# Optimization experiments

Hardware: AMD Instinct MI355X
Metric: run time of the kernel (lower is better)

Reference implementation:

```python
import jax, jax.numpy as jnp
import numpy as np

D = 768
H = 12
B, T = 2, 2048


def _layernorm(x, g, b, eps=1e-5):
    m = jnp.mean(x, axis=-1, keepdims=True)
    v = jnp.mean((x - m) ** 2, axis=-1, keepdims=True)
    return (x - m) * jax.lax.rsqrt(v + eps) * g + b


def setup_inputs() -> dict:
    key = jax.random.key(0)
    ks = jax.random.split(key, 10)
    s = 0.02
    return {
        "x": jax.random.normal(ks[0], (B, T, D), dtype=jnp.float32),
        "attn_mask": jnp.ones((B, T), dtype=jnp.int32),
        "Wq": jax.random.normal(ks[1], (D, D), dtype=jnp.float32) * s,
        "Wk": jax.random.normal(ks[2], (D, D), dtype=jnp.float32) * s,
        "Wv": jax.random.normal(ks[3], (D, D), dtype=jnp.float32) * s,
        "Wo": jax.random.normal(ks[4], (D, D), dtype=jnp.float32) * s,
        "bo": jnp.zeros((D,), dtype=jnp.float32),
        "ln1_g": jnp.ones((D,), dtype=jnp.float32),
        "ln1_b": jnp.zeros((D,), dtype=jnp.float32),
        "ln2_g": jnp.ones((D,), dtype=jnp.float32),
        "ln2_b": jnp.zeros((D,), dtype=jnp.float32),
        "W1": jax.random.normal(ks[5], (D, 4 * D), dtype=jnp.float32) * s,
        "b1": jnp.zeros((4 * D,), dtype=jnp.float32),
        "W2": jax.random.normal(ks[6], (4 * D, D), dtype=jnp.float32) * s,
        "b2": jnp.zeros((D,), dtype=jnp.float32),
    }


def reference(x, attn_mask, Wq, Wk, Wv, Wo, bo, ln1_g, ln1_b, ln2_g, ln2_b, W1, b1, W2, b2):
    d = x.shape[-1]
    hs = d // H
    # --- multi-head self-attention on ln1(x) ---
    h = _layernorm(x, ln1_g, ln1_b)
    q = jnp.einsum("btd,dhk->bhtk", h, Wq.reshape(d, H, hs))
    k = jnp.einsum("btd,dhk->bhtk", h, Wk.reshape(d, H, hs))
    v = jnp.einsum("btd,dhk->bhtk", h, Wv.reshape(d, H, hs))
    # NOTE: original scales by embed_dim**-0.5 (C = embed_dim), not head_size
    scores = jnp.einsum("bhtk,bhsk->bhts", q, k) * (d ** -0.5)
    key_mask = (attn_mask == 0)[:, None, None, :]  # [B,1,1,T] over key dim
    scores = jnp.where(key_mask, -jnp.inf, scores)
    wei = jax.nn.softmax(scores, axis=-1)
    out = jnp.einsum("bhts,bhsk->bhtk", wei, v)
    out = out.transpose(0, 2, 1, 3).reshape(x.shape)  # concat heads -> [B,T,D]
    x = x + out @ Wo + bo
    # --- feed-forward on ln2(x) ---
    h2 = _layernorm(x, ln2_g, ln2_b)
    ff = jax.nn.relu(h2 @ W1 + b1) @ W2 + b2
    return x + ff
```

## Files before the change

kernel.cpp:

```cpp
#include <hip/hip_runtime.h>
#include <hip/hip_bf16.h>


typedef unsigned short u16;
typedef unsigned int u32;
typedef __attribute__((ext_vector_type(8))) short s16x8;
typedef __attribute__((ext_vector_type(4))) short s16x4;
typedef __attribute__((ext_vector_type(4))) float fx4;

#define D_MODEL 768
#define NH 12
#define HS 64
#define TT 2048
#define BB 2

__device__ __forceinline__ u16 f2bf(float f) {
  union { float f; u32 u; } v; v.f = f;
  u32 r = v.u + 0x7fffu + ((v.u >> 16) & 1u);
  return (u16)(r >> 16);
}
__device__ __forceinline__ float bf2f(u16 h) {
  union { u32 u; float f; } v; v.u = ((u32)h) << 16; return v.f;
}
__device__ __forceinline__ s16x4 pack4(float a, float b, float c, float d) {
  union { __hip_bfloat162 h2[2]; s16x4 v; } u;
  u.h2[0] = __float22bfloat162_rn({a, b});
  u.h2[1] = __float22bfloat162_rn({c, d});
  return u.v;
}

__device__ __forceinline__ void async16(const void* g, void* l) {
  __builtin_amdgcn_global_load_lds(
      (const __attribute__((address_space(1))) u32*)g,
      (__attribute__((address_space(3))) u32*)l, 16, 0, 0);
}

__device__ __forceinline__ s16x4 lds_rd64(const u16* base, int row, int g) {
  int a = row * 64 + ((((g >> 1) ^ (row & 7)) << 3) | ((g & 1) << 2));
  return *(const s16x4*)(base + a);
}

__global__ __launch_bounds__(256) void tconv(const float* __restrict__ in,
                                             u16* __restrict__ out, int R, int C) {
  __shared__ float t[32][33];
  int c0 = blockIdx.x * 32, r0 = blockIdx.y * 32;
  int x = threadIdx.x, y = threadIdx.y;
  for (int i = 0; i < 4; i++)
    t[y + i * 8][x] = in[(size_t)(r0 + y + i * 8) * C + c0 + x];
  __syncthreads();
  for (int i = 0; i < 4; i++)
    out[(size_t)(c0 + y + i * 8) * R + r0 + x] = f2bf(t[x][y + i * 8]);
}

__global__ __launch_bounds__(256) void tconv3(const float* __restrict__ w0,
                                              const float* __restrict__ w1,
                                              const float* __restrict__ w2,
                                              u16* __restrict__ out) {
  __shared__ float t[32][33];
  const float* in = blockIdx.z == 0 ? w0 : blockIdx.z == 1 ? w1 : w2;
  u16* o = out + (size_t)blockIdx.z * 768 * 768;
  int c0 = blockIdx.x * 32, r0 = blockIdx.y * 32;
  int x = threadIdx.x, y = threadIdx.y;
  for (int i = 0; i < 4; i++)
    t[y + i * 8][x] = in[(size_t)(r0 + y + i * 8) * 768 + c0 + x];
  __syncthreads();
  for (int i = 0; i < 4; i++)
    o[(size_t)(c0 + y + i * 8) * 768 + r0 + x] = f2bf(t[x][y + i * 8]);
}

__global__ __launch_bounds__(256) void vt_extract(const u16* __restrict__ qkv,
                                                  u16* __restrict__ vt) {
  __shared__ u16 t[32][33];
  int bh = blockIdx.z, b = bh / NH, h = bh % NH;
  int t0 = blockIdx.x * 32, v0 = blockIdx.y * 32;
  int x = threadIdx.x, y = threadIdx.y;
  for (int i = 0; i < 4; i++)
    t[y + i * 8][x] = qkv[(size_t)(b * TT + t0 + y + i * 8) * 2304 + 1536 + h * HS + v0 + x];
  __syncthreads();
  for (int i = 0; i < 4; i++)
    vt[(size_t)(bh * HS + v0 + y + i * 8) * TT + t0 + x] = t[x][y + i * 8];
}

__global__ __launch_bounds__(256) void maskbias(const int* __restrict__ mask,
                                                float* __restrict__ mb) {
  int i = blockIdx.x * 256 + threadIdx.x;
  mb[i] = mask[i] ? 0.f : -1e30f;
}

__global__ __launch_bounds__(256) void ln_kernel(const float* __restrict__ x,
                                                 const float* __restrict__ g,
                                                 const float* __restrict__ bta,
                                                 u16* __restrict__ out) {
  int row = blockIdx.x;
  const float* xr = x + (size_t)row * D_MODEL;
  int tid = threadIdx.x;
  float v0 = xr[tid], v1 = xr[tid + 256], v2 = xr[tid + 512];
  float s = v0 + v1 + v2, sq = v0 * v0 + v1 * v1 + v2 * v2;
  for (int m = 1; m < 64; m <<= 1) { s += __shfl_xor(s, m); sq += __shfl_xor(sq, m); }
  __shared__ float ss[4], ssq[4];
  int w = tid >> 6;
  if ((tid & 63) == 0) { ss[w] = s; ssq[w] = sq; }
  __syncthreads();
  s = ss[0] + ss[1] + ss[2] + ss[3];
  sq = ssq[0] + ssq[1] + ssq[2] + ssq[3];
  float mean = s * (1.f / D_MODEL);
  float var = sq * (1.f / D_MODEL) - mean * mean;
  float rstd = rsqrtf(var + 1e-5f);
  u16* orow = out + (size_t)row * D_MODEL;
  orow[tid]       = f2bf((v0 - mean) * rstd * g[tid]       + bta[tid]);
  orow[tid + 256] = f2bf((v1 - mean) * rstd * g[tid + 256] + bta[tid + 256]);
  orow[tid + 512] = f2bf((v2 - mean) * rstd * g[tid + 512] + bta[tid + 512]);
}

__global__ __launch_bounds__(256) void red_wo_ln(
    const u16* __restrict__ p0, const u16* __restrict__ p1,
    const u16* __restrict__ p2, const u16* __restrict__ p3,
    const float* __restrict__ x, const float* __restrict__ bo,
    const float* __restrict__ g, const float* __restrict__ be,
    float* __restrict__ yv, u16* __restrict__ h2) {
  int row = blockIdx.x, tid = threadIdx.x;
  size_t base = (size_t)row * D_MODEL;
  float v[3];
  float s = 0.f, sq = 0.f;
  for (int i = 0; i < 3; i++) {
    int c = tid + i * 256;
    size_t idx = base + c;
    float t = bf2f(p0[idx]) + bf2f(p1[idx]) + bf2f(p2[idx]) + bf2f(p3[idx])
            + x[idx] + bo[c];
    v[i] = t; yv[idx] = t;
    s += t; sq += t * t;
  }
  for (int m = 1; m < 64; m <<= 1) { s += __shfl_xor(s, m); sq += __shfl_xor(sq, m); }
  __shared__ float ss[4], ssq[4];
  int w = tid >> 6;
  if ((tid & 63) == 0) { ss[w] = s; ssq[w] = sq; }
  __syncthreads();
  s = ss[0] + ss[1] + ss[2] + ss[3];
  sq = ssq[0] + ssq[1] + ssq[2] + ssq[3];
  float mean = s * (1.f / D_MODEL);
  float var = sq * (1.f / D_MODEL) - mean * mean;
  float rstd = rsqrtf(var + 1e-5f);
  for (int i = 0; i < 3; i++) {
    int c = tid + i * 256;
    h2[base + c] = f2bf((v[i] - mean) * rstd * g[c] + be[c]);
  }
}

__global__ __launch_bounds__(256) void red_ff2(
    const u16* __restrict__ p0, const u16* __restrict__ p1,
    const u16* __restrict__ p2, const float* __restrict__ yv,
    const float* __restrict__ bias, float* __restrict__ out) {
  size_t i = ((size_t)blockIdx.x * 256 + threadIdx.x) * 4;
  int col = (int)(i % D_MODEL);
  ushort4 a = *(const ushort4*)(p0 + i);
  ushort4 b = *(const ushort4*)(p1 + i);
  ushort4 c = *(const ushort4*)(p2 + i);
  float4 y = *(const float4*)(yv + i);
  float4 o;
  o.x = bf2f(a.x) + bf2f(b.x) + bf2f(c.x) + y.x + bias[col];
  o.y = bf2f(a.y) + bf2f(b.y) + bf2f(c.y) + y.y + bias[col + 1];
  o.z = bf2f(a.z) + bf2f(b.z) + bf2f(c.z) + y.z + bias[col + 2];
  o.w = bf2f(a.w) + bf2f(b.w) + bf2f(c.w) + y.w + bias[col + 3];
  *(float4*)(out + i) = o;
}

template <int EPI>
__global__ __launch_bounds__(256) void gemm_bt(
    const u16* __restrict__ A, const u16* __restrict__ Bt,
    int M, int N, int K,
    u16* __restrict__ outb, const float* __restrict__ bias,
    float qs, int qn,
    u16* __restrict__ p0, u16* __restrict__ p1,
    u16* __restrict__ p2, u16* __restrict__ p3) {
  __shared__ __align__(16) u16 lA[128 * 32];
  __shared__ __align__(16) u16 lB[128 * 32];
  const int tid = threadIdx.x;
  const int lane = tid & 63, w = tid >> 6;
  const int quad = lane >> 4, l15 = lane & 15;
  const int wm = w >> 1, wn = w & 1;
  const int bm = blockIdx.y, bn = blockIdx.x;
  const int Ksub = K / gridDim.z;
  const int k0 = blockIdx.z * Ksub;

  fx4 acc[4][4] = {};

  for (int kt = k0; kt < k0 + Ksub; kt += 32) {
    __syncthreads();
    for (int t = 0; t < 2; t++) {
      int p = (w * 2 + t) * 64 + lane;
      int m = p >> 2, qp = p & 3;
      int ql = qp ^ ((m >> 1) & 3);
      async16(A + (size_t)(bm * 128 + m) * K + kt + ql * 8,
              (char*)lA + (w * 2 + t) * 1024);
    }
    for (int t = 0; t < 2; t++) {
      int p = (w * 2 + t) * 64 + lane;
      int n = p >> 2, qp = p & 3;
      int ql = qp ^ ((n >> 1) & 3);
      async16(Bt + (size_t)(bn * 128 + n) * K + kt + ql * 8,
              (char*)lB + (w * 2 + t) * 1024);
    }
    __syncthreads();
    s16x8 af[4], bfr[4];
    for (int i = 0; i < 4; i++) {
      int m = wm * 64 + i * 16 + l15;
      int phys = m * 4 + (quad ^ ((m >> 1) & 3));
      af[i] = *(const s16x8*)((const char*)lA + phys * 16);
    }
    for (int j = 0; j < 4; j++) {
      int n = wn * 64 + j * 16 + l15;
      int phys = n * 4 + (quad ^ ((n >> 1) & 3));
      bfr[j] = *(const s16x8*)((const char*)lB + phys * 16);
    }
    for (int i = 0; i < 4; i++)
      for (int j = 0; j < 4; j++)
        acc[i][j] = __builtin_amdgcn_mfma_f32_16x16x32_bf16(af[i], bfr[j], acc[i][j], 0, 0, 0);
  }

  u16* pb = nullptr;
  if (EPI == 3)
    pb = blockIdx.z == 0 ? p0 : blockIdx.z == 1 ? p1 : blockIdx.z == 2 ? p2 : p3;

  for (int i = 0; i < 4; i++)
    for (int j = 0; j < 4; j++)
      for (int r = 0; r < 4; r++) {
        int row = bm * 128 + wm * 64 + i * 16 + quad * 4 + r;
        int col = bn * 128 + wn * 64 + j * 16 + l15;
        float v = acc[i][j][r];
        if (EPI == 0) {
          float vv = (col < qn) ? v * qs : v;
          outb[(size_t)row * N + col] = f2bf(vv);
        } else if (EPI == 2) {
          outb[(size_t)row * N + col] = f2bf(fmaxf(v + bias[col], 0.f));
        } else {
          pb[(size_t)row * N + col] = f2bf(v);
        }
      }
}

__global__ __launch_bounds__(256) void attn_kernel(
    const u16* __restrict__ qkv, const u16* __restrict__ vt,
    const float* __restrict__ maskadd,
    u16* __restrict__ pO0, u16* __restrict__ pO1, float* __restrict__ pL) {
  __shared__ __align__(16) u16 sQ[64 * 64];
  __shared__ __align__(16) u16 sK[64 * 64];
  __shared__ __align__(16) u16 sV[64 * 64];
  __shared__ __align__(16) float smask[1024];
  const int bh = blockIdx.y, b = bh / NH, h = bh % NH;
  const int qt = blockIdx.x, sp = blockIdx.z;
  const int tid = threadIdx.x, lane = tid & 63, w = tid >> 6;
  const int quad = lane >> 4, l15 = lane & 15;

  for (int t = 0; t < 2; t++) {
    int p = (w * 2 + t) * 64 + lane;
    int m = p >> 3, qp = p & 7, ql = qp ^ (m & 7);
    async16(qkv + (size_t)(b * TT + qt * 64 + m) * 2304 + h * HS + ql * 8,
            (char*)sQ + (w * 2 + t) * 1024);
  }
  for (int j = 0; j < 4; j++)
    smask[tid + j * 256] = maskadd[b * TT + sp * 1024 + tid + j * 256];
  __syncthreads();

  s16x4 qb[4];
  for (int ks = 0; ks < 4; ks++)
    qb[ks] = lds_rd64(sQ, w * 16 + l15, ks * 4 + quad);

  float lsum = 0.f;
  fx4 o[4] = {};

  for (int kc = 0; kc < 16; kc++) {
    int key0 = sp * 1024 + kc * 64;
    __syncthreads();
    for (int t = 0; t < 2; t++) {
      int p = (w * 2 + t) * 64 + lane;
      int m = p >> 3, qp = p & 7, ql = qp ^ (m & 7);
      async16(qkv + (size_t)(b * TT + key0 + m) * 2304 + D_MODEL + h * HS + ql * 8,
              (char*)sK + (w * 2 + t) * 1024);
    }
    for (int t = 0; t < 2; t++) {
      int p = (w * 2 + t) * 64 + lane;
      int m = p >> 3, qp = p & 7, ql = qp ^ (m & 7);
      async16(vt + (size_t)bh * HS * TT + (size_t)m * TT + key0 + ql * 8,
              (char*)sV + (w * 2 + t) * 1024);
    }
    __syncthreads();

    for (int kt = 0; kt < 4; kt++) {
      float4 mb = *(const float4*)&smask[kc * 64 + kt * 16 + quad * 4];
      fx4 s = {mb.x, mb.y, mb.z, mb.w};
      for (int ks = 0; ks < 4; ks++) {
        s16x4 ak = lds_rd64(sK, kt * 16 + l15, ks * 4 + quad);
        s = __builtin_amdgcn_mfma_f32_16x16x16bf16_1k(ak, qb[ks], s, 0, 0, 0);
      }
      float e0 = __builtin_amdgcn_exp2f(s[0]);
      float e1 = __builtin_amdgcn_exp2f(s[1]);
      float e2 = __builtin_amdgcn_exp2f(s[2]);
      float e3 = __builtin_amdgcn_exp2f(s[3]);
      lsum += (e0 + e1) + (e2 + e3);
      s16x4 pB = pack4(e0, e1, e2, e3);
      for (int jv = 0; jv < 4; jv++) {
        s16x4 av = lds_rd64(sV, jv * 16 + l15, kt * 4 + quad);
        o[jv] = __builtin_amdgcn_mfma_f32_16x16x16bf16_1k(av, pB, o[jv], 0, 0, 0);
      }
    }
  }

  lsum += __shfl_xor(lsum, 16);
  lsum += __shfl_xor(lsum, 32);

  const int tile = bh * 32 + qt;
  u16* po = sp ? pO1 : pO0;
  size_t base = (size_t)tile * 4096;
  for (int jv = 0; jv < 4; jv++)
    for (int r = 0; r < 4; r++) {
      int vd = jv * 16 + quad * 4 + r;
      po[base + vd * 64 + w * 16 + l15] = f2bf(o[jv][r]);
    }
  if (quad == 0) pL[sp * 49152 + tile * 64 + w * 16 + l15] = lsum;
}

__global__ __launch_bounds__(256) void attn_reduce(
    const u16* __restrict__ pO0, const u16* __restrict__ pO1,
    const float* __restrict__ pL, u16* __restrict__ out) {
  __shared__ float T[64 * 65];
  __shared__ float rinv[64];
  const int tile = blockIdx.x;
  const int bh = tile >> 5, qt = tile & 31, b = bh / NH, h = bh % NH;
  const int t = threadIdx.x;
  if (t < 64) rinv[t] = 1.f / (pL[tile * 64 + t] + pL[49152 + tile * 64 + t]);
  __syncthreads();
  size_t base = (size_t)tile * 4096;
  for (int i = 0; i < 16; i++) {
    int idx = i * 256 + t, vd = idx >> 6, q = idx & 63;
    T[vd * 65 + q] = (bf2f(pO0[base + idx]) + bf2f(pO1[base + idx])) * rinv[q];
  }
  __syncthreads();
  int q = t >> 2, vb = (t & 3) * 16;
  u16* orow = out + (size_t)(b * TT + qt * 64 + q) * D_MODEL + h * HS + vb;
  for (int i = 0; i < 8; i++) {
    int vd = vb + i * 2;
    u32 pk = (u32)f2bf(T[vd * 65 + q]) | ((u32)f2bf(T[(vd + 1) * 65 + q]) << 16);
    *(u32*)(orow + i * 2) = pk;
  }
}

extern "C" void kernel_launch(void* const* d_in, const int* in_sizes, int n_in,
                              void* d_out, int out_size, void* d_ws, size_t ws_size,
                              hipStream_t stream) {
  const float* x    = (const float*)d_in[0];
  const int*   mask = (const int*)d_in[1];
  const float* Wq   = (const float*)d_in[2];
  const float* Wk   = (const float*)d_in[3];
  const float* Wv   = (const float*)d_in[4];
  const float* Wo   = (const float*)d_in[5];
  const float* bo   = (const float*)d_in[6];
  const float* g1   = (const float*)d_in[7];
  const float* be1  = (const float*)d_in[8];
  const float* g2   = (const float*)d_in[9];
  const float* be2  = (const float*)d_in[10];
  const float* W1   = (const float*)d_in[11];
  const float* bb1  = (const float*)d_in[12];
  const float* W2   = (const float*)d_in[13];
  const float* bb2  = (const float*)d_in[14];
  float* out = (float*)d_out;
  char* ws = (char*)d_ws;

  u16*   WqkvT = (u16*)(ws + 0);
  u16*   WoT   = (u16*)(ws + 3538944);
  u16*   W1T   = (u16*)(ws + 4718592);
  u16*   W2T   = (u16*)(ws + 9437184);
  u16*   h1    = (u16*)(ws + 14155776);
  u16*   QKV   = (u16*)(ws + 20447232);
  u16*   Vt    = (u16*)(ws + 39321600);
  u16*   attn  = (u16*)(ws + 45613056);
  float* yv    = (float*)(ws + 51904512);
  float* mbias = yv;
  u16*   pO0   = h1;
  u16*   pO1   = (u16*)(ws + 51920896);
  float* pL    = (float*)(ws + 58212352);
  u16*   h2    = h1;
  u16*   ff1   = QKV;
  u16* pw0 = (u16*)(ws + 20447232);
  u16* pw1 = (u16*)(ws + 26738688);
  u16* pw2 = (u16*)(ws + 33030144);
  u16* pw3 = (u16*)(ws + 39321600);
  u16* pf0 = (u16*)(ws + 0);
  u16* pf1 = (u16*)(ws + 14155776);
  u16* pf2 = (u16*)(ws + 45613056);

  const float QS = 0.05205875399f;

  dim3 tb(32, 8);
  tconv3<<<dim3(24, 24, 3), tb, 0, stream>>>(Wq, Wk, Wv, WqkvT);
  tconv<<<dim3(24, 24), tb, 0, stream>>>(Wo, WoT, 768, 768);
  tconv<<<dim3(96, 24), tb, 0, stream>>>(W1, W1T, 768, 3072);
  tconv<<<dim3(24, 96), tb, 0, stream>>>(W2, W2T, 3072, 768);
  maskbias<<<16, 256, 0, stream>>>(mask, mbias);

  ln_kernel<<<4096, 256, 0, stream>>>(x, g1, be1, h1);
  gemm_bt<0><<<dim3(18, 32, 1), 256, 0, stream>>>(h1, WqkvT, 4096, 2304, 768,
      QKV, nullptr, QS, 768, nullptr, nullptr, nullptr, nullptr);
  vt_extract<<<dim3(64, 2, 24), tb, 0, stream>>>(QKV, Vt);
  attn_kernel<<<dim3(32, 24, 2), 256, 0, stream>>>(QKV, Vt, mbias, pO0, pO1, pL);
  attn_reduce<<<768, 256, 0, stream>>>(pO0, pO1, pL, attn);
  gemm_bt<3><<<dim3(6, 32, 4), 256, 0, stream>>>(attn, WoT, 4096, 768, 768,
      nullptr, nullptr, 1.f, 0, pw0, pw1, pw2, pw3);
  red_wo_ln<<<4096, 256, 0, stream>>>(pw0, pw1, pw2, pw3, x, bo, g2, be2, yv, h2);
  gemm_bt<2><<<dim3(24, 32, 1), 256, 0, stream>>>(h2, W1T, 4096, 3072, 768,
      ff1, bb1, 1.f, 0, nullptr, nullptr, nullptr, nullptr);
  gemm_bt<3><<<dim3(6, 32, 3), 256, 0, stream>>>(ff1, W2T, 4096, 768, 3072,
      nullptr, nullptr, 1.f, 0, pf0, pf1, pf2, nullptr);
  red_ff2<<<3072, 256, 0, stream>>>(pf0, pf1, pf2, yv, bb2, out);
}
```

Measured before the change: 323.7 us.

## Widen attention blocks to 128 queries with register-prefetched V and 16x16x32 MFMA

Each attention block now has 8 waves and covers 128 query rows instead of 64, so every K/V tile loaded into LDS is reused by twice as many waves. The QK^T product uses the 16x16x32 bf16 MFMA with 8-element reads. V is prefetched one chunk ahead into registers and written to a padded LDS tile instead of going through async global-to-LDS copies. In exchange the kernel launches half as many blocks, uses more registers per block, and the V store adds an LDS write step to each iteration.

```diff
diff --git a/kernel.cpp b/kernel.cpp
--- a/kernel.cpp
+++ b/kernel.cpp
@@ -33,11 +33,6 @@
   __builtin_amdgcn_global_load_lds(
       (const __attribute__((address_space(1))) u32*)g,
       (__attribute__((address_space(3))) u32*)l, 16, 0, 0);
-}
-
-__device__ __forceinline__ s16x4 lds_rd64(const u16* base, int row, int g) {
-  int a = row * 64 + ((((g >> 1) ^ (row & 7)) << 3) | ((g & 1) << 2));
-  return *(const s16x4*)(base + a);
 }
 
 __global__ __launch_bounds__(256) void tconv(const float* __restrict__ in,
@@ -238,85 +233,91 @@
       }
 }
 
-__global__ __launch_bounds__(256) void attn_kernel(
+__global__ __launch_bounds__(512) void attn_kernel(
     const u16* __restrict__ qkv, const u16* __restrict__ vt,
     const float* __restrict__ maskadd,
     u16* __restrict__ pO0, u16* __restrict__ pO1, float* __restrict__ pL) {
-  __shared__ __align__(16) u16 sQ[64 * 64];
+  __shared__ __align__(16) u16 sQ[128 * 64];
   __shared__ __align__(16) u16 sK[64 * 64];
-  __shared__ __align__(16) u16 sV[64 * 64];
+  __shared__ __align__(16) u16 sV[64 * 68];
   __shared__ __align__(16) float smask[1024];
   const int bh = blockIdx.y, b = bh / NH, h = bh % NH;
   const int qt = blockIdx.x, sp = blockIdx.z;
   const int tid = threadIdx.x, lane = tid & 63, w = tid >> 6;
   const int quad = lane >> 4, l15 = lane & 15;
 
-  for (int t = 0; t < 2; t++) {
-    int p = (w * 2 + t) * 64 + lane;
+  for (int i = 0; i < 2; i++) {
+    int p = i * 512 + tid;
     int m = p >> 3, qp = p & 7, ql = qp ^ (m & 7);
-    async16(qkv + (size_t)(b * TT + qt * 64 + m) * 2304 + h * HS + ql * 8,
-            (char*)sQ + (w * 2 + t) * 1024);
-  }
-  for (int j = 0; j < 4; j++)
-    smask[tid + j * 256] = maskadd[b * TT + sp * 1024 + tid + j * 256];
-  __syncthreads();
-
-  s16x4 qb[4];
-  for (int ks = 0; ks < 4; ks++)
-    qb[ks] = lds_rd64(sQ, w * 16 + l15, ks * 4 + quad);
+    async16(qkv + (size_t)(b * TT + qt * 128 + m) * 2304 + h * HS + ql * 8,
+            (char*)sQ + i * 8192 + w * 1024);
+  }
+  smask[tid]       = maskadd[b * TT + sp * 1024 + tid];
+  smask[tid + 512] = maskadd[b * TT + sp * 1024 + 512 + tid];
+  const u16* vbase = vt + (size_t)bh * HS * TT + (size_t)(tid >> 3) * TT + sp * 1024;
+  s16x8 vcur = *(const s16x8*)(vbase + (tid & 7) * 8);
+  __syncthreads();
+
+  const int qrow = w * 16 + l15;
+  s16x8 aq0 = *(const s16x8*)((const char*)sQ + qrow * 128 + ((quad ^ (l15 & 7)) * 16));
+  s16x8 aq1 = *(const s16x8*)((const char*)sQ + qrow * 128 + (((4 + quad) ^ (l15 & 7)) * 16));
+
+  const char* pK0 = (const char*)sK + l15 * 128 + ((quad ^ (l15 & 7)) * 16);
+  const char* pK1 = (const char*)sK + l15 * 128 + (((4 + quad) ^ (l15 & 7)) * 16);
+  const char* pV  = (const char*)sV + l15 * 136 + quad * 8;
+  char* vwr = (char*)sV + (tid >> 3) * 136 + (tid & 7) * 16;
 
   float lsum = 0.f;
   fx4 o[4] = {};
 
   for (int kc = 0; kc < 16; kc++) {
-    int key0 = sp * 1024 + kc * 64;
     __syncthreads();
-    for (int t = 0; t < 2; t++) {
-      int p = (w * 2 + t) * 64 + lane;
-      int m = p >> 3, qp = p & 7, ql = qp ^ (m & 7);
-      async16(qkv + (size_t)(b * TT + key0 + m) * 2304 + D_MODEL + h * HS + ql * 8,
-              (char*)sK + (w * 2 + t) * 1024);
-    }
-    for (int t = 0; t < 2; t++) {
-      int p = (w * 2 + t) * 64 + lane;
-      int m = p >> 3, qp = p & 7, ql = qp ^ (m & 7);
-      async16(vt + (size_t)bh * HS * TT + (size_t)m * TT + key0 + ql * 8,
-              (char*)sV + (w * 2 + t) * 1024);
-    }
+    {
+      int m = tid >> 3, qp = tid & 7, ql = qp ^ (m & 7);
+      async16(qkv + (size_t)(b * TT + sp * 1024 + kc * 64 + m) * 2304 + D_MODEL + h * HS + ql * 8,
+              (char*)sK + w * 1024);
+    }
+    *(s16x8*)vwr = vcur;
     __syncthreads();
-
+    int kn = (kc < 15) ? (kc + 1) * 64 : kc * 64;
+    s16x8 vnxt = *(const s16x8*)(vbase + kn + (tid & 7) * 8);
+
+    #pragma unroll
     for (int kt = 0; kt < 4; kt++) {
       float4 mb = *(const float4*)&smask[kc * 64 + kt * 16 + quad * 4];
       fx4 s = {mb.x, mb.y, mb.z, mb.w};
-      for (int ks = 0; ks < 4; ks++) {
-        s16x4 ak = lds_rd64(sK, kt * 16 + l15, ks * 4 + quad);
-        s = __builtin_amdgcn_mfma_f32_16x16x16bf16_1k(ak, qb[ks], s, 0, 0, 0);
-      }
+      s16x8 ak0 = *(const s16x8*)(pK0 + kt * 2048);
+      s16x8 ak1 = *(const s16x8*)(pK1 + kt * 2048);
+      s = __builtin_amdgcn_mfma_f32_16x16x32_bf16(ak0, aq0, s, 0, 0, 0);
+      s = __builtin_amdgcn_mfma_f32_16x16x32_bf16(ak1, aq1, s, 0, 0, 0);
       float e0 = __builtin_amdgcn_exp2f(s[0]);
       float e1 = __builtin_amdgcn_exp2f(s[1]);
       float e2 = __builtin_amdgcn_exp2f(s[2]);
       float e3 = __builtin_amdgcn_exp2f(s[3]);
       lsum += (e0 + e1) + (e2 + e3);
       s16x4 pB = pack4(e0, e1, e2, e3);
+      #pragma unroll
       for (int jv = 0; jv < 4; jv++) {
-        s16x4 av = lds_rd64(sV, jv * 16 + l15, kt * 4 + quad);
+        s16x4 av = *(const s16x4*)(pV + jv * 2176 + kt * 32);
         o[jv] = __builtin_amdgcn_mfma_f32_16x16x16bf16_1k(av, pB, o[jv], 0, 0, 0);
       }
     }
+    vcur = vnxt;
   }
 
   lsum += __shfl_xor(lsum, 16);
   lsum += __shfl_xor(lsum, 32);
 
-  const int tile = bh * 32 + qt;
+  const int tile = bh * 32 + qt * 2 + (w >> 2);
+  const int sub = (w & 3) * 16;
   u16* po = sp ? pO1 : pO0;
   size_t base = (size_t)tile * 4096;
   for (int jv = 0; jv < 4; jv++)
     for (int r = 0; r < 4; r++) {
       int vd = jv * 16 + quad * 4 + r;
-      po[base + vd * 64 + w * 16 + l15] = f2bf(o[jv][r]);
-    }
-  if (quad == 0) pL[sp * 49152 + tile * 64 + w * 16 + l15] = lsum;
+      po[base + vd * 64 + sub + l15] = f2bf(o[jv][r]);
+    }
+  if (quad == 0) pL[sp * 49152 + tile * 64 + sub + l15] = lsum;
 }
 
 __global__ __launch_bounds__(256) void attn_reduce(
@@ -401,7 +402,7 @@
   gemm_bt<0><<<dim3(18, 32, 1), 256, 0, stream>>>(h1, WqkvT, 4096, 2304, 768,
       QKV, nullptr, QS, 768, nullptr, nullptr, nullptr, nullptr);
   vt_extract<<<dim3(64, 2, 24), tb, 0, stream>>>(QKV, Vt);
-  attn_kernel<<<dim3(32, 24, 2), 256, 0, stream>>>(QKV, Vt, mbias, pO0, pO1, pL);
+  attn_kernel<<<dim3(16, 24, 2), 512, 0, stream>>>(QKV, Vt, mbias, pO0, pO1, pL);
   attn_reduce<<<768, 256, 0, stream>>>(pO0, pO1, pL, attn);
   gemm_bt<3><<<dim3(6, 32, 4), 256, 0, stream>>>(attn, WoT, 4096, 768, 768,
       nullptr, nullptr, 1.f, 0, pw0, pw1, pw2, pw3);
```

Result: faster. 301.8 us (-6.8%).
